# Kernel optimization log

Measured on AMD Instinct MI355X. Metric: run time of the kernel, lower is better.

## Reference

```python
import jax, jax.numpy as jnp
import numpy as np

N = 2048; E = 5; C = 2; W_IN = 256; W_OUT = 128; NUM_CLASS = 8; NT = 1024


def _norm(H, add):
    # faithful to GTN.norm: transpose, zero diagonal, (optionally add I),
    # row-degree-normalize (diag(deg^-1) @ H expressed as row scaling), transpose back
    Ht = H.T
    n = Ht.shape[0]
    eye = jnp.eye(n, dtype=Ht.dtype)
    Ht = Ht * (1.0 - eye)
    if add:
        Ht = Ht + eye
    deg = jnp.sum(Ht, axis=1)
    deg_inv = jnp.where(deg == 0, jnp.zeros_like(deg), 1.0 / deg)
    return (deg_inv[:, None] * Ht).T


def _gtconv(A_e, w):
    # A_e: [E, N, N]; w: [C, E]; softmax over edge types then weighted sum
    return jnp.einsum('ce,enm->cnm', jax.nn.softmax(w, axis=1), A_e)


def setup_inputs() -> dict:
    key = jax.random.key(0)
    ks = jax.random.split(key, 12)
    A = jax.random.uniform(ks[0], (N, N, E), dtype=jnp.float32)
    X = jax.random.uniform(ks[1], (N, W_IN), dtype=jnp.float32)  # BCE target, in [0,1]
    target_x = jax.random.randint(ks[2], (NT,), 0, N)
    target = jax.random.randint(ks[3], (NT,), 0, NUM_CLASS)
    w0a = 0.1 * jax.random.normal(ks[4], (C, E), dtype=jnp.float32)
    w0b = 0.1 * jax.random.normal(ks[5], (C, E), dtype=jnp.float32)
    w1a = 0.1 * jax.random.normal(ks[6], (C, E), dtype=jnp.float32)
    W = jax.random.normal(ks[7], (W_IN, W_OUT), dtype=jnp.float32) * (1.0 / np.sqrt(W_IN))
    W1 = jax.random.normal(ks[8], (W_OUT * C, W_OUT), dtype=jnp.float32) * (1.0 / np.sqrt(W_OUT * C))
    W2 = jax.random.normal(ks[9], (W_OUT * C, W_IN), dtype=jnp.float32) * (1.0 / np.sqrt(W_OUT * C))
    lin_w = jax.random.normal(ks[10], (NUM_CLASS, W_OUT), dtype=jnp.float32) * (1.0 / np.sqrt(W_OUT))
    lin_b = jnp.zeros((NUM_CLASS,), dtype=jnp.float32)
    return {"A": A, "X": X, "W": W, "W1": W1, "W2": W2, "lin_w": lin_w,
            "lin_b": lin_b, "w0a": w0a, "w0b": w0b, "w1a": w1a,
            "target_x": target_x, "target": target}


def reference(A, X, W, W1, W2, lin_w, lin_b, w0a, w0b, w1a, target_x, target):
    A_e = jnp.transpose(A, (2, 0, 1))          # [E, N, N]
    # layer 0 (first=True): H = conv1(A) @ conv2(A)
    a = _gtconv(A_e, w0a)                      # [C, N, N]
    b = _gtconv(A_e, w0b)
    H = jnp.einsum('cij,cjk->cik', a, b)
    # layer 1 (first=False): H = normalization(H) @ conv1(A)
    Hn = jax.vmap(lambda h: _norm(h, False))(H)
    a1 = _gtconv(A_e, w1a)
    H = jnp.einsum('cij,cjk->cik', Hn, a1)
    # per-channel GCN conv: relu(norm(H_c, add=True).T @ (X @ W)), concat on features
    XW = X @ W                                 # [N, w_out]
    Hn2 = jax.vmap(lambda h: _norm(h, True))(H)
    Xc = jax.nn.relu(jnp.einsum('cji,jd->cid', Hn2, XW))  # [C, N, w_out]
    n = X.shape[0]
    X_cat = jnp.transpose(Xc, (1, 0, 2)).reshape(n, -1)   # [N, C*w_out]
    # sum channels, then the two head GCN convs share norm(H_sum, add=True)
    Hs = _norm(jnp.sum(H, axis=0), True)
    X_r = Hs.T @ (X_cat @ W2)                  # [N, w_in]
    X_o = Hs.T @ (X_cat @ W1)                  # [N, w_out]
    y = X_o[target_x] @ lin_w.T + lin_b        # [NT, num_class]
    # clamp reconstruction into [0,1] via sigmoid on out-of-range entries
    X_r = jnp.where(X_r > 1, jax.nn.sigmoid(X_r), X_r)
    X_r = jnp.where(X_r < 0, jax.nn.sigmoid(X_r), X_r)
    p = jnp.clip(X_r, 1e-7, 1.0 - 1e-7)
    lossR = -jnp.mean(X * jnp.log(p) + (1.0 - X) * jnp.log1p(-p))
    logp = jax.nn.log_softmax(y, axis=-1)
    lossC = -jnp.mean(jnp.take_along_axis(logp, target[:, None], axis=1))
    loss = lossC + lossR
    Ws = (jax.lax.stop_gradient(jax.nn.softmax(w0a, axis=1)),
          jax.lax.stop_gradient(jax.nn.softmax(w0b, axis=1)),
          jax.lax.stop_gradient(jax.nn.softmax(w1a, axis=1)))
    return (loss, y, Ws, lossR)
```

## Files before the change

### kernel.cpp

```cpp
#include <hip/hip_runtime.h>
#include <hip/hip_bf16.h>
#include <math.h>

#define NDIM 2048
#define EDIM 5
#define CDIM 2
#define WIN 256
#define WOUT 128
#define NCLS 8
#define NTGT 1024
#define NN ((size_t)NDIM * NDIM)
#define HNSC 256.0f
#define HNSCI 0.00390625f

typedef __attribute__((ext_vector_type(8))) short short8v;
typedef __attribute__((ext_vector_type(4))) float float4v;
typedef __attribute__((ext_vector_type(8))) int int8v;
typedef __attribute__((ext_vector_type(4))) int int4v;
typedef __attribute__((ext_vector_type(2))) int int2v;

__device__ __forceinline__ void gl2lds16(const void* g, void* l) {
  __builtin_amdgcn_global_load_lds((__attribute__((address_space(1))) const unsigned int*)g,
                                   (__attribute__((address_space(3))) unsigned int*)l, 16, 0, 0);
}
__device__ __forceinline__ float bf2f(unsigned short u) {
  return __uint_as_float(((unsigned)u) << 16);
}
__device__ __forceinline__ unsigned short f2bf(float f) {
  __hip_bfloat16 h = __float2bfloat16(f);
  return *(unsigned short*)&h;
}
__device__ __forceinline__ unsigned char f2fp8(float f) {
  return (unsigned char)(__builtin_amdgcn_cvt_pk_fp8_f32(f, f, 0, false) & 0xff);
}

#define N_XC (CDIM * NDIM * WOUT)
#define N_XO (NDIM * 384)
#define N_W12 (2 * WOUT * 384)
#define N_PREP (N_XC + N_XO + N_W12 + CDIM * NDIM + 16 + 30)
__global__ __launch_bounds__(256) void wsum_mega_k(
    const float* __restrict__ A, const float* __restrict__ w0a,
    const float* __restrict__ w0b, const float* __restrict__ w1a,
    unsigned char* __restrict__ a_out, unsigned char* __restrict__ bT,
    unsigned char* __restrict__ a1T,
    float* __restrict__ acc, float* __restrict__ deg,
    float* __restrict__ XcPre, float* __restrict__ XoXr, float* __restrict__ W12,
    const float* __restrict__ W1, const float* __restrict__ W2,
    float* __restrict__ dout) {
  const int b = blockIdx.x;
  const int tid = threadIdx.x;
  if (b >= 4096) {
    int idx = (b - 4096) * 256 + tid;
    if (idx < N_XC) { XcPre[idx] = 0.f; return; }
    idx -= N_XC;
    if (idx < N_XO) { XoXr[idx] = 0.f; return; }
    idx -= N_XO;
    if (idx < N_W12) {
      int k = idx / 384, j = idx - k * 384;
      W12[idx] = (j < 128) ? W1[k * 128 + j] : W2[k * 256 + (j - 128)];
      return;
    }
    idx -= N_W12;
    if (idx < CDIM * NDIM) { deg[idx] = 0.f; return; }
    idx -= CDIM * NDIM;
    if (idx < 16) { acc[idx] = 0.f; return; }
    idx -= 16;
    if (idx < 30) {
      int m = idx / 10, rr = idx - m * 10, c = rr / 5, e = rr - c * 5;
      const float* src = (m == 0) ? w0a : (m == 1) ? w0b : w1a;
      float mx = -1e30f;
      for (int t = 0; t < 5; ++t) mx = fmaxf(mx, src[c * 5 + t]);
      float s = 0.f, ve = 0.f;
      for (int t = 0; t < 5; ++t) {
        float ex = expf(src[c * 5 + t] - mx);
        s += ex;
        if (t == e) ve = ex;
      }
      dout[1 + NTGT * NCLS + idx] = ve / s;
    }
    return;
  }
  __shared__ float swl[32];
  __shared__ float tb[CDIM][32][33];
  __shared__ float tc[CDIM][32][33];
  if (tid < 6) {
    int m = tid >> 1, c = tid & 1;
    const float* src = (m == 0) ? w0a : (m == 1) ? w0b : w1a;
    float mx = -1e30f;
    for (int e = 0; e < 5; ++e) mx = fmaxf(mx, src[c * 5 + e]);
    float ex[5]; float s = 0.f;
    for (int e = 0; e < 5; ++e) { ex[e] = expf(src[c * 5 + e] - mx); s += ex[e]; }
    for (int e = 0; e < 5; ++e) swl[m * 10 + c * 5 + e] = ex[e] / s;
  }
  __syncthreads();
  const int bx = (b & 63) * 32, by = (b >> 6) * 32;
  const int tx = tid & 31, ty = tid >> 5;
#pragma unroll
  for (int rr = 0; rr < 32; rr += 8) {
    int n = by + ty + rr, m = bx + tx;
    size_t base = ((size_t)n * NDIM + m) * EDIM;
    float v0 = A[base], v1 = A[base + 1], v2 = A[base + 2], v3 = A[base + 3], v4 = A[base + 4];
#pragma unroll
    for (int c = 0; c < CDIM; ++c) {
      float sa = swl[c*5]*v0 + swl[c*5+1]*v1 + swl[c*5+2]*v2 + swl[c*5+3]*v3 + swl[c*5+4]*v4;
      float sb = swl[10+c*5]*v0 + swl[10+c*5+1]*v1 + swl[10+c*5+2]*v2 + swl[10+c*5+3]*v3 + swl[10+c*5+4]*v4;
      float sc = swl[20+c*5]*v0 + swl[20+c*5+1]*v1 + swl[20+c*5+2]*v2 + swl[20+c*5+3]*v3 + swl[20+c*5+4]*v4;
      a_out[c * NN + (size_t)n * NDIM + m] = f2fp8(sa);
      tb[c][ty + rr][tx] = sb;
      tc[c][ty + rr][tx] = sc;
    }
  }
  __syncthreads();
#pragma unroll
  for (int rr = 0; rr < 32; rr += 8) {
    int mm = bx + ty + rr, nn2 = by + tx;
#pragma unroll
    for (int c = 0; c < CDIM; ++c) {
      bT[c * NN + (size_t)mm * NDIM + nn2] = f2fp8(tb[c][tx][ty + rr]);
      a1T[c * NN + (size_t)mm * NDIM + nn2] = f2fp8(tc[c][tx][ty + rr]);
    }
  }
}

__global__ __launch_bounds__(256) void mfma_fp8_k(
    const unsigned char* __restrict__ Ab, const unsigned char* __restrict__ Bt,
    __hip_bfloat16* __restrict__ Cv, int K, int ldc,
    size_t sA, size_t sB, size_t sC, float* __restrict__ cs) {
  __shared__ __align__(16) unsigned char As[128 * 128];
  __shared__ __align__(16) unsigned char Bs[128 * 128];
  const int tid = threadIdx.x;
  const int lane = tid & 63;
  const int wave = tid >> 6;
  const int batch = blockIdx.z;
  const unsigned char* A = Ab + (size_t)batch * sA;
  const unsigned char* B = Bt + (size_t)batch * sB;
  const int row0 = blockIdx.y * 128;
  const int col0 = blockIdx.x * 128;

  const int wr = (wave >> 1) * 64;
  const int wc = (wave & 1) * 64;
  const int q = lane >> 4;
  const int r = lane & 15;

  float4v acc[4][4] = {};

  const int srow = lane >> 3;
  const int scol = ((lane & 7) ^ (srow & 7)) * 16;
  const int fsw = r & 7;

  for (int k0 = 0; k0 < K; k0 += 128) {
    __syncthreads();
#pragma unroll
    for (int s = 0; s < 4; ++s) {
      gl2lds16(A + (size_t)(row0 + s * 32 + wave * 8 + srow) * K + k0 + scol,
               As + s * 4096 + wave * 1024);
      gl2lds16(B + (size_t)(col0 + s * 32 + wave * 8 + srow) * K + k0 + scol,
               Bs + s * 4096 + wave * 1024);
    }
    __syncthreads();

    union { int8v v; int4v h[2]; } ua[4], ub[4];
#pragma unroll
    for (int i = 0; i < 4; ++i) {
      const unsigned char* pa = As + (size_t)(wr + i * 16 + r) * 128;
      const unsigned char* pb = Bs + (size_t)(wc + i * 16 + r) * 128;
      ua[i].h[0] = *(const int4v*)(pa + (((2 * q) ^ fsw) * 16));
      ua[i].h[1] = *(const int4v*)(pa + (((2 * q + 1) ^ fsw) * 16));
      ub[i].h[0] = *(const int4v*)(pb + (((2 * q) ^ fsw) * 16));
      ub[i].h[1] = *(const int4v*)(pb + (((2 * q + 1) ^ fsw) * 16));
    }
#pragma unroll
    for (int i = 0; i < 4; ++i)
#pragma unroll
      for (int j = 0; j < 4; ++j)
        acc[i][j] = __builtin_amdgcn_mfma_scale_f32_16x16x128_f8f6f4(
            ua[i].v, ub[j].v, acc[i][j], 0, 0, 0, 0x7F7F7F7F, 0, 0x7F7F7F7F);
  }

  __hip_bfloat16* Cp = Cv + (size_t)batch * sC;
#pragma unroll
  for (int i = 0; i < 4; ++i) {
    int row = row0 + wr + i * 16 + q * 4;
#pragma unroll
    for (int j = 0; j < 4; ++j) {
      int col = col0 + wc + j * 16 + r;
#pragma unroll
      for (int e = 0; e < 4; ++e)
        Cp[(size_t)(row + e) * ldc + col] = __float2bfloat16(acc[i][j][e]);
    }
  }

  if (cs) {
    float* csp = cs + (size_t)batch * NDIM;
#pragma unroll
    for (int j = 0; j < 4; ++j) {
      int col = col0 + wc + j * 16 + r;
      float s = 0.f;
#pragma unroll
      for (int i = 0; i < 4; ++i) {
        int rowb = row0 + wr + i * 16 + q * 4;
#pragma unroll
        for (int e = 0; e < 4; ++e)
          if (rowb + e != col) s += acc[i][j][e];
      }
      s += __shfl_xor(s, 16, 64);
      s += __shfl_xor(s, 32, 64);
      if (lane < 16) atomicAdd(&csp[col], s);
    }
  }
}

__global__ __launch_bounds__(256) void mfma_bt_k(
    const __hip_bfloat16* __restrict__ Ab, const __hip_bfloat16* __restrict__ Bt,
    float* __restrict__ Cv, int K, int ldc,
    size_t sA, size_t sB, size_t sC, int nsplit) {
  __shared__ __hip_bfloat16 As[128 * 64];
  __shared__ __hip_bfloat16 Bs[128 * 64];
  const int tid = threadIdx.x;
  const int lane = tid & 63;
  const int wave = tid >> 6;
  const int batch = blockIdx.z / nsplit;
  const int split = blockIdx.z - batch * nsplit;
  const __hip_bfloat16* A = Ab + (size_t)batch * sA;
  const __hip_bfloat16* B = Bt + (size_t)batch * sB;
  const int row0 = blockIdx.y * 128;
  const int col0 = blockIdx.x * 128;
  const int kchunk = K / nsplit;
  const int kbeg = split * kchunk;
  const int kend = kbeg + kchunk;

  const int wr = (wave >> 1) * 64;
  const int wc = (wave & 1) * 64;
  const int q = lane >> 4;
  const int r = lane & 15;

  float4v acc[4][4] = {};

  const int srow = lane >> 3;
  const int scol = ((lane & 7) ^ (srow & 7)) * 8;
  const int fsw = r & 7;

  for (int k0 = kbeg; k0 < kend; k0 += 64) {
    __syncthreads();
#pragma unroll
    for (int s = 0; s < 4; ++s) {
      gl2lds16(A + (size_t)(row0 + s * 32 + wave * 8 + srow) * K + k0 + scol,
               (char*)As + s * 4096 + wave * 1024);
      gl2lds16(B + (size_t)(col0 + s * 32 + wave * 8 + srow) * K + k0 + scol,
               (char*)Bs + s * 4096 + wave * 1024);
    }
    __syncthreads();
#pragma unroll
    for (int h = 0; h < 2; ++h) {
      short8v af[4], bf[4];
#pragma unroll
      for (int i = 0; i < 4; ++i) {
        af[i] = *(const short8v*)((const char*)As + (size_t)(wr + i * 16 + r) * 128 +
                                  (((h * 4 + q) ^ fsw) * 16));
        bf[i] = *(const short8v*)((const char*)Bs + (size_t)(wc + i * 16 + r) * 128 +
                                  (((h * 4 + q) ^ fsw) * 16));
      }
#pragma unroll
      for (int i = 0; i < 4; ++i)
#pragma unroll
        for (int j = 0; j < 4; ++j)
          acc[i][j] = __builtin_amdgcn_mfma_f32_16x16x32_bf16(af[i], bf[j], acc[i][j], 0, 0, 0);
    }
  }

  float* Cp = Cv + (size_t)batch * sC;
#pragma unroll
  for (int i = 0; i < 4; ++i) {
    int row = row0 + wr + i * 16 + q * 4;
#pragma unroll
    for (int j = 0; j < 4; ++j) {
      int col = col0 + wc + j * 16 + r;
#pragma unroll
      for (int e = 0; e < 4; ++e) {
        float v = acc[i][j][e];
        if (nsplit > 1) atomicAdd(&Cp[(size_t)(row + e) * ldc + col], v);
        else Cp[(size_t)(row + e) * ldc + col] = v;
      }
    }
  }
}

__global__ __launch_bounds__(256) void col_scale_k(const __hip_bfloat16* __restrict__ H,
                                                   const float* __restrict__ deg,
                                                   unsigned char* __restrict__ out) {
  size_t base = ((size_t)blockIdx.x * 256 + threadIdx.x) * 8;
  int c = (int)(base >> 22);
  int i = (int)((base >> 11) & (NDIM - 1));
  int j0 = (int)(base & (NDIM - 1));
  union { short8v v; unsigned short u[8]; } p;
  p.v = *(const short8v*)(H + base);
  float f[8];
#pragma unroll
  for (int t = 0; t < 8; ++t) {
    int j = j0 + t;
    float d = deg[c * NDIM + j];
    float inv = (d == 0.f) ? 0.f : HNSC / d;
    float v = (i == j) ? 0.f : bf2f(p.u[t]);
    f[t] = v * inv;
  }
  int w0 = __builtin_amdgcn_cvt_pk_fp8_f32(f[0], f[1], 0, false);
  w0 = __builtin_amdgcn_cvt_pk_fp8_f32(f[2], f[3], w0, true);
  int w1 = __builtin_amdgcn_cvt_pk_fp8_f32(f[4], f[5], 0, false);
  w1 = __builtin_amdgcn_cvt_pk_fp8_f32(f[6], f[7], w1, true);
  int2v o; o.x = w0; o.y = w1;
  *(int2v*)(out + base) = o;
}

__global__ __launch_bounds__(256) void rowmega_k(const __hip_bfloat16* __restrict__ H1T,
                                                 __hip_bfloat16* __restrict__ Hn2T,
                                                 __hip_bfloat16* __restrict__ HsT) {
  const int m = blockIdx.x;
  const int tid = threadIdx.x;
  const size_t rb = (size_t)m * NDIM + tid * 8;
  union { short8v v; unsigned short u[8]; } a0, a1;
  a0.v = *(const short8v*)(H1T + rb);
  a1.v = *(const short8v*)(H1T + NN + rb);
  float v0[8], v1[8];
  float s0 = 0.f, s1 = 0.f;
#pragma unroll
  for (int t = 0; t < 8; ++t) {
    v0[t] = bf2f(a0.u[t]) * HNSCI;
    v1[t] = bf2f(a1.u[t]) * HNSCI;
    s0 += v0[t]; s1 += v1[t];
  }
  __shared__ float ds[2];
  __shared__ float red[2][4];
  __shared__ float bc[3];
  if (tid == (m >> 3)) { ds[0] = v0[m & 7]; ds[1] = v1[m & 7]; }
  for (int off = 32; off > 0; off >>= 1) {
    s0 += __shfl_down(s0, off, 64);
    s1 += __shfl_down(s1, off, 64);
  }
  if ((tid & 63) == 0) { red[0][tid >> 6] = s0; red[1][tid >> 6] = s1; }
  __syncthreads();
  if (tid == 0) {
    float t0 = red[0][0] + red[0][1] + red[0][2] + red[0][3];
    float t1 = red[1][0] + red[1][1] + red[1][2] + red[1][3];
    float r0 = t0 - ds[0] + 1.f;
    float r1 = t1 - ds[1] + 1.f;
    float rs = t0 + t1 - ds[0] - ds[1] + 1.f;
    bc[0] = (r0 == 0.f) ? 0.f : 1.f / r0;
    bc[1] = (r1 == 0.f) ? 0.f : 1.f / r1;
    bc[2] = (rs == 0.f) ? 0.f : 1.f / rs;
  }
  __syncthreads();
  float i0 = bc[0], i1 = bc[1], is = bc[2];
  union { short8v v; unsigned short u[8]; } o0, o1, os;
#pragma unroll
  for (int t = 0; t < 8; ++t) {
    bool dg = (tid * 8 + t == m);
    o0.u[t] = f2bf((dg ? 1.f : v0[t]) * i0);
    o1.u[t] = f2bf((dg ? 1.f : v1[t]) * i1);
    os.u[t] = f2bf((dg ? 1.f : (v0[t] + v1[t])) * is);
  }
  *(short8v*)(Hn2T + rb) = o0.v;
  *(short8v*)(Hn2T + NN + rb) = o1.v;
  *(short8v*)(HsT + rb) = os.v;
}

#define TS 64
#define BK 16
__global__ __launch_bounds__(256) void sgemm_tb_k(const float* __restrict__ A,
                                                  const float* __restrict__ B,
                                                  __hip_bfloat16* __restrict__ Dt,
                                                  int K, int lda, int ldb, int ldt,
                                                  int amode) {
  __shared__ float As[BK][TS];
  __shared__ float Bs[BK][TS + 4];
  const int tid = threadIdx.x;
  const int brow = blockIdx.y * TS;
  const int bcol = blockIdx.x * TS;
  const int tx = tid & 15;
  const int ty = tid >> 4;
  const int la_r = tid >> 2;
  const int la_k = (tid & 3) << 2;
  const int lb_k = tid >> 4;
  const int lb_c = (tid & 15) << 2;
  float acc[4][4] = {{0.f}};
  for (int k0 = 0; k0 < K; k0 += BK) {
    float4 av;
    if (amode == 0) {
      av = *(const float4*)(A + (size_t)(brow + la_r) * lda + k0 + la_k);
    } else {
      int k = k0 + la_k;
      const float* ap = A + (size_t)(k >> 7) * ((size_t)NDIM * WOUT) +
                        (size_t)(brow + la_r) * WOUT + (k & 127);
      av = *(const float4*)ap;
      av.x = fmaxf(av.x, 0.f); av.y = fmaxf(av.y, 0.f);
      av.z = fmaxf(av.z, 0.f); av.w = fmaxf(av.w, 0.f);
    }
    float4 bv = *(const float4*)(B + (size_t)(k0 + lb_k) * ldb + bcol + lb_c);
    __syncthreads();
    As[la_k + 0][la_r] = av.x;
    As[la_k + 1][la_r] = av.y;
    As[la_k + 2][la_r] = av.z;
    As[la_k + 3][la_r] = av.w;
    *(float4*)&Bs[lb_k][lb_c] = bv;
    __syncthreads();
#pragma unroll
    for (int kk = 0; kk < BK; ++kk) {
      float a0 = As[kk][ty * 4 + 0], a1 = As[kk][ty * 4 + 1];
      float a2 = As[kk][ty * 4 + 2], a3 = As[kk][ty * 4 + 3];
      float b0 = Bs[kk][tx * 4 + 0], b1 = Bs[kk][tx * 4 + 1];
      float b2 = Bs[kk][tx * 4 + 2], b3 = Bs[kk][tx * 4 + 3];
      acc[0][0] += a0 * b0; acc[0][1] += a0 * b1; acc[0][2] += a0 * b2; acc[0][3] += a0 * b3;
      acc[1][0] += a1 * b0; acc[1][1] += a1 * b1; acc[1][2] += a1 * b2; acc[1][3] += a1 * b3;
      acc[2][0] += a2 * b0; acc[2][1] += a2 * b1; acc[2][2] += a2 * b2; acc[2][3] += a2 * b3;
      acc[3][0] += a3 * b0; acc[3][1] += a3 * b1; acc[3][2] += a3 * b2; acc[3][3] += a3 * b3;
    }
  }
#pragma unroll
  for (int i = 0; i < 4; ++i)
#pragma unroll
    for (int j = 0; j < 4; ++j)
      Dt[(size_t)(bcol + tx * 4 + j) * ldt + brow + ty * 4 + i] = __float2bfloat16(acc[i][j]);
}

__global__ __launch_bounds__(256) void loss_mega_k(const float* __restrict__ XoXr,
                                                   const float* __restrict__ X,
                                                   const float* __restrict__ lin_w,
                                                   const float* __restrict__ lin_b,
                                                   const int* __restrict__ txs,
                                                   const int* __restrict__ tgt,
                                                   float* __restrict__ yout,
                                                   float* __restrict__ acc) {
  const int b = blockIdx.x;
  const int tid = threadIdx.x;
  if (b < 2048) {
    float xr = XoXr[(size_t)b * 384 + 128 + tid];
    if (xr > 1.f) xr = 1.f / (1.f + expf(-xr));
    if (xr < 0.f) xr = 1.f / (1.f + expf(-xr));
    float p = fminf(fmaxf(xr, 1e-7f), 1.f - 1e-7f);
    float xv = X[(size_t)b * WIN + tid];
    float t = xv * logf(p) + (1.f - xv) * log1pf(-p);
    for (int off = 32; off > 0; off >>= 1) t += __shfl_down(t, off, 64);
    __shared__ float red[4];
    if ((tid & 63) == 0) red[tid >> 6] = t;
    __syncthreads();
    if (tid == 0) atomicAdd(acc + 1, red[0] + red[1] + red[2] + red[3]);
    return;
  }
  const int t = b - 2048;
  __shared__ float xo[WOUT];
  __shared__ float ys[NCLS];
  int x = txs[t];
  if (tid < WOUT) xo[tid] = XoXr[(size_t)x * 384 + tid];
  __syncthreads();
  if (tid < NCLS) {
    float s = lin_b[tid];
    for (int d = 0; d < WOUT; ++d) s += xo[d] * lin_w[tid * WOUT + d];
    ys[tid] = s;
    yout[(size_t)t * NCLS + tid] = s;
  }
  __syncthreads();
  if (tid == 0) {
    float m = ys[0];
    for (int k = 1; k < NCLS; ++k) m = fmaxf(m, ys[k]);
    float se = 0.f;
    for (int k = 0; k < NCLS; ++k) se += expf(ys[k] - m);
    float lse = m + logf(se);
    atomicAdd(acc, lse - ys[tgt[t]]);
  }
}

__global__ void finalize_k(const float* __restrict__ acc, float* __restrict__ dout) {
  float lossC = acc[0] / (float)NTGT;
  float lossR = -acc[1] / (float)(NDIM * WIN);
  dout[0] = lossC + lossR;
  dout[1 + NTGT * NCLS + 30] = lossR;
}

extern "C" void kernel_launch(void* const* d_in, const int* in_sizes, int n_in,
                              void* d_out, int out_size, void* d_ws, size_t ws_size,
                              hipStream_t stream) {
  const float* A    = (const float*)d_in[0];
  const float* X    = (const float*)d_in[1];
  const float* W    = (const float*)d_in[2];
  const float* W1   = (const float*)d_in[3];
  const float* W2   = (const float*)d_in[4];
  const float* linw = (const float*)d_in[5];
  const float* linb = (const float*)d_in[6];
  const float* w0a  = (const float*)d_in[7];
  const float* w0b  = (const float*)d_in[8];
  const float* w1a  = (const float*)d_in[9];
  const int* txs    = (const int*)d_in[10];
  const int* tgt    = (const int*)d_in[11];
  float* dout = (float*)d_out;

  float* ws = (float*)d_ws;
  unsigned char* wb = (unsigned char*)d_ws;
  unsigned char* P_a   = wb;
  unsigned char* P_bT  = wb + 2 * NN;
  unsigned char* P_a1T = wb + 4 * NN;
  unsigned char* P_Hn  = wb + 6 * NN;
  __hip_bfloat16* H_bf   = (__hip_bfloat16*)(ws + 2 * NN);
  __hip_bfloat16* H1T_bf = (__hip_bfloat16*)(ws + 3 * NN);
  __hip_bfloat16* Hn2T   = (__hip_bfloat16*)(ws + 4 * NN);
  __hip_bfloat16* HsT    = (__hip_bfloat16*)(ws);
  float* sm   = ws + 5 * NN;
  float* acc   = sm;                 sm += 16;
  float* deg   = sm;                 sm += CDIM * NDIM;
  __hip_bfloat16* XWT = (__hip_bfloat16*)sm;    sm += (size_t)NDIM * WOUT / 2;
  float* XcPre = sm;                 sm += (size_t)CDIM * NDIM * WOUT;
  float* W12   = sm;                 sm += (size_t)(2 * WOUT) * 384;
  __hip_bfloat16* XC12T = (__hip_bfloat16*)sm;  sm += (size_t)NDIM * 384 / 2;
  float* XoXr  = sm;                 sm += (size_t)NDIM * 384;

  dim3 blk256(256);

  wsum_mega_k<<<dim3(4096 + (N_PREP + 255) / 256), blk256, 0, stream>>>(
      A, w0a, w0b, w1a, P_a, P_bT, P_a1T, acc, deg, XcPre, XoXr, W12, W1, W2, dout);
  mfma_fp8_k<<<dim3(16, 16, 2), blk256, 0, stream>>>(P_a, P_bT, H_bf, NDIM, NDIM,
                                                     NN, NN, NN, deg);
  col_scale_k<<<dim3((unsigned)(2 * NN / 2048)), blk256, 0, stream>>>(H_bf, deg, P_Hn);
  mfma_fp8_k<<<dim3(16, 16, 2), blk256, 0, stream>>>(P_a1T, P_Hn, H1T_bf, NDIM, NDIM,
                                                     NN, NN, NN, nullptr);
  rowmega_k<<<dim3(NDIM), blk256, 0, stream>>>(H1T_bf, Hn2T, HsT);
  sgemm_tb_k<<<dim3(WOUT / TS, NDIM / TS), blk256, 0, stream>>>(X, W, XWT, WIN,
                                                                WIN, WOUT, NDIM, 0);
  mfma_bt_k<<<dim3(1, 16, 16), blk256, 0, stream>>>(Hn2T, XWT, XcPre, NDIM, WOUT,
                                                    NN, 0, (size_t)NDIM * WOUT, 8);
  sgemm_tb_k<<<dim3(384 / TS, NDIM / TS), blk256, 0, stream>>>(XcPre, W12, XC12T, 2 * WOUT,
                                                               0, 384, NDIM, 1);
  mfma_bt_k<<<dim3(3, 16, 8), blk256, 0, stream>>>(HsT, XC12T, XoXr, NDIM, 384,
                                                   0, 0, 0, 8);
  loss_mega_k<<<dim3(2048 + NTGT), blk256, 0, stream>>>(XoXr, X, linw, linb, txs, tgt,
                                                        dout + 1, acc);
  finalize_k<<<dim3(1), dim3(1), 0, stream>>>(acc, dout);
}
```

Baseline: 341.7 us.

## Replace fp32 SIMT GEMMs with bf16 MFMA and split-K partial buffers

The two small fp32 SIMT GEMMs (X@W and Xcat@W12) are replaced by the bf16 MFMA kernel, with operands converted and transposed to bf16 in the prep kernel. Split-K results are written to separate per-split partial buffers instead of atomically added, so consumers (a new reduce+relu kernel and the loss kernel) sum the partials. This removes the float atomics and the zero-init passes. In exchange it adds an extra kernel launch, extra partial-buffer traffic, and bf16 rounding of X and the weights.

```diff
diff --git a/kernel.cpp b/kernel.cpp
--- a/kernel.cpp
+++ b/kernel.cpp
@@ -34,33 +34,39 @@
   return (unsigned char)(__builtin_amdgcn_cvt_pk_fp8_f32(f, f, 0, false) & 0xff);
 }
 
-#define N_XC (CDIM * NDIM * WOUT)
-#define N_XO (NDIM * 384)
-#define N_W12 (2 * WOUT * 384)
-#define N_PREP (N_XC + N_XO + N_W12 + CDIM * NDIM + 16 + 30)
+#define N_XBF (NDIM * WIN)
+#define N_WT (WIN * WOUT)
+#define N_W12T (384 * WIN)
+#define N_PREP (N_XBF + N_WT + N_W12T + CDIM * NDIM + 16 + 30)
 __global__ __launch_bounds__(256) void wsum_mega_k(
     const float* __restrict__ A, const float* __restrict__ w0a,
     const float* __restrict__ w0b, const float* __restrict__ w1a,
     unsigned char* __restrict__ a_out, unsigned char* __restrict__ bT,
     unsigned char* __restrict__ a1T,
     float* __restrict__ acc, float* __restrict__ deg,
-    float* __restrict__ XcPre, float* __restrict__ XoXr, float* __restrict__ W12,
+    const float* __restrict__ X, const float* __restrict__ W,
     const float* __restrict__ W1, const float* __restrict__ W2,
+    __hip_bfloat16* __restrict__ Xbf, __hip_bfloat16* __restrict__ WTbf,
+    __hip_bfloat16* __restrict__ W12Tbf,
     float* __restrict__ dout) {
   const int b = blockIdx.x;
   const int tid = threadIdx.x;
   if (b >= 4096) {
     int idx = (b - 4096) * 256 + tid;
-    if (idx < N_XC) { XcPre[idx] = 0.f; return; }
-    idx -= N_XC;
-    if (idx < N_XO) { XoXr[idx] = 0.f; return; }
-    idx -= N_XO;
-    if (idx < N_W12) {
-      int k = idx / 384, j = idx - k * 384;
-      W12[idx] = (j < 128) ? W1[k * 128 + j] : W2[k * 256 + (j - 128)];
+    if (idx < N_XBF) { Xbf[idx] = __float2bfloat16(X[idx]); return; }
+    idx -= N_XBF;
+    if (idx < N_WT) {
+      int d = idx >> 8, k = idx & 255;
+      WTbf[idx] = __float2bfloat16(W[k * WOUT + d]);
       return;
     }
-    idx -= N_W12;
+    idx -= N_WT;
+    if (idx < N_W12T) {
+      int j = idx >> 8, k = idx & 255;
+      W12Tbf[idx] = __float2bfloat16(j < 128 ? W1[k * 128 + j] : W2[k * 256 + (j - 128)]);
+      return;
+    }
+    idx -= N_W12T;
     if (idx < CDIM * NDIM) { deg[idx] = 0.f; return; }
     idx -= CDIM * NDIM;
     if (idx < 16) { acc[idx] = 0.f; return; }
@@ -212,8 +218,8 @@
 
 __global__ __launch_bounds__(256) void mfma_bt_k(
     const __hip_bfloat16* __restrict__ Ab, const __hip_bfloat16* __restrict__ Bt,
-    float* __restrict__ Cv, int K, int ldc,
-    size_t sA, size_t sB, size_t sC, int nsplit) {
+    void* __restrict__ Cv, int K, int ldc,
+    size_t sA, size_t sB, size_t sC, size_t sSplit, int nsplit, int mode) {
   __shared__ __hip_bfloat16 As[128 * 64];
   __shared__ __hip_bfloat16 Bs[128 * 64];
   const int tid = threadIdx.x;
@@ -268,18 +274,30 @@
     }
   }
 
-  float* Cp = Cv + (size_t)batch * sC;
-#pragma unroll
-  for (int i = 0; i < 4; ++i) {
-    int row = row0 + wr + i * 16 + q * 4;
-#pragma unroll
-    for (int j = 0; j < 4; ++j) {
-      int col = col0 + wc + j * 16 + r;
-#pragma unroll
-      for (int e = 0; e < 4; ++e) {
-        float v = acc[i][j][e];
-        if (nsplit > 1) atomicAdd(&Cp[(size_t)(row + e) * ldc + col], v);
-        else Cp[(size_t)(row + e) * ldc + col] = v;
+  if (mode == 1) {
+    __hip_bfloat16* Cp = (__hip_bfloat16*)Cv + (size_t)batch * sC;
+#pragma unroll
+    for (int i = 0; i < 4; ++i) {
+      int row = row0 + wr + i * 16 + q * 4;
+#pragma unroll
+      for (int j = 0; j < 4; ++j) {
+        int col = col0 + wc + j * 16 + r;
+#pragma unroll
+        for (int e = 0; e < 4; ++e)
+          Cp[(size_t)(row + e) * ldc + col] = __float2bfloat16(acc[i][j][e]);
+      }
+    }
+  } else {
+    float* Cp = (float*)Cv + (size_t)batch * sC + (size_t)split * sSplit;
+#pragma unroll
+    for (int i = 0; i < 4; ++i) {
+      int row = row0 + wr + i * 16 + q * 4;
+#pragma unroll
+      for (int j = 0; j < 4; ++j) {
+        int col = col0 + wc + j * 16 + r;
+#pragma unroll
+        for (int e = 0; e < 4; ++e)
+          Cp[(size_t)(row + e) * ldc + col] = acc[i][j][e];
       }
     }
   }
@@ -363,65 +381,20 @@
   *(short8v*)(HsT + rb) = os.v;
 }
 
-#define TS 64
-#define BK 16
-__global__ __launch_bounds__(256) void sgemm_tb_k(const float* __restrict__ A,
-                                                  const float* __restrict__ B,
-                                                  __hip_bfloat16* __restrict__ Dt,
-                                                  int K, int lda, int ldb, int ldt,
-                                                  int amode) {
-  __shared__ float As[BK][TS];
-  __shared__ float Bs[BK][TS + 4];
-  const int tid = threadIdx.x;
-  const int brow = blockIdx.y * TS;
-  const int bcol = blockIdx.x * TS;
-  const int tx = tid & 15;
-  const int ty = tid >> 4;
-  const int la_r = tid >> 2;
-  const int la_k = (tid & 3) << 2;
-  const int lb_k = tid >> 4;
-  const int lb_c = (tid & 15) << 2;
-  float acc[4][4] = {{0.f}};
-  for (int k0 = 0; k0 < K; k0 += BK) {
-    float4 av;
-    if (amode == 0) {
-      av = *(const float4*)(A + (size_t)(brow + la_r) * lda + k0 + la_k);
-    } else {
-      int k = k0 + la_k;
-      const float* ap = A + (size_t)(k >> 7) * ((size_t)NDIM * WOUT) +
-                        (size_t)(brow + la_r) * WOUT + (k & 127);
-      av = *(const float4*)ap;
-      av.x = fmaxf(av.x, 0.f); av.y = fmaxf(av.y, 0.f);
-      av.z = fmaxf(av.z, 0.f); av.w = fmaxf(av.w, 0.f);
-    }
-    float4 bv = *(const float4*)(B + (size_t)(k0 + lb_k) * ldb + bcol + lb_c);
-    __syncthreads();
-    As[la_k + 0][la_r] = av.x;
-    As[la_k + 1][la_r] = av.y;
-    As[la_k + 2][la_r] = av.z;
-    As[la_k + 3][la_r] = av.w;
-    *(float4*)&Bs[lb_k][lb_c] = bv;
-    __syncthreads();
-#pragma unroll
-    for (int kk = 0; kk < BK; ++kk) {
-      float a0 = As[kk][ty * 4 + 0], a1 = As[kk][ty * 4 + 1];
-      float a2 = As[kk][ty * 4 + 2], a3 = As[kk][ty * 4 + 3];
-      float b0 = Bs[kk][tx * 4 + 0], b1 = Bs[kk][tx * 4 + 1];
-      float b2 = Bs[kk][tx * 4 + 2], b3 = Bs[kk][tx * 4 + 3];
-      acc[0][0] += a0 * b0; acc[0][1] += a0 * b1; acc[0][2] += a0 * b2; acc[0][3] += a0 * b3;
-      acc[1][0] += a1 * b0; acc[1][1] += a1 * b1; acc[1][2] += a1 * b2; acc[1][3] += a1 * b3;
-      acc[2][0] += a2 * b0; acc[2][1] += a2 * b1; acc[2][2] += a2 * b2; acc[2][3] += a2 * b3;
-      acc[3][0] += a3 * b0; acc[3][1] += a3 * b1; acc[3][2] += a3 * b2; acc[3][3] += a3 * b3;
-    }
-  }
-#pragma unroll
-  for (int i = 0; i < 4; ++i)
-#pragma unroll
-    for (int j = 0; j < 4; ++j)
-      Dt[(size_t)(bcol + tx * 4 + j) * ldt + brow + ty * 4 + i] = __float2bfloat16(acc[i][j]);
-}
-
-__global__ __launch_bounds__(256) void loss_mega_k(const float* __restrict__ XoXr,
+__global__ __launch_bounds__(256) void reduce_relu_k(const float* __restrict__ P7,
+                                                     __hip_bfloat16* __restrict__ Xcat) {
+  int idx = blockIdx.x * 256 + threadIdx.x;
+  int c = idx >> 18;
+  int rem = idx & 262143;
+  float s = 0.f;
+#pragma unroll
+  for (int sp = 0; sp < 8; ++sp)
+    s += P7[(size_t)c * 2097152 + (size_t)sp * 262144 + rem];
+  int n = rem >> 7, d = rem & 127;
+  Xcat[(size_t)n * 256 + (c << 7) + d] = __float2bfloat16(fmaxf(s, 0.f));
+}
+
+__global__ __launch_bounds__(256) void loss_mega_k(const float* __restrict__ P10,
                                                    const float* __restrict__ X,
                                                    const float* __restrict__ lin_w,
                                                    const float* __restrict__ lin_b,
@@ -432,7 +405,10 @@
   const int b = blockIdx.x;
   const int tid = threadIdx.x;
   if (b < 2048) {
-    float xr = XoXr[(size_t)b * 384 + 128 + tid];
+    float xr = 0.f;
+#pragma unroll
+    for (int sp = 0; sp < 8; ++sp)
+      xr += P10[(size_t)sp * 786432 + (size_t)b * 384 + 128 + tid];
     if (xr > 1.f) xr = 1.f / (1.f + expf(-xr));
     if (xr < 0.f) xr = 1.f / (1.f + expf(-xr));
     float p = fminf(fmaxf(xr, 1e-7f), 1.f - 1e-7f);
@@ -449,7 +425,13 @@
   __shared__ float xo[WOUT];
   __shared__ float ys[NCLS];
   int x = txs[t];
-  if (tid < WOUT) xo[tid] = XoXr[(size_t)x * 384 + tid];
+  if (tid < WOUT) {
+    float s = 0.f;
+#pragma unroll
+    for (int sp = 0; sp < 8; ++sp)
+      s += P10[(size_t)sp * 786432 + (size_t)x * 384 + tid];
+    xo[tid] = s;
+  }
   __syncthreads();
   if (tid < NCLS) {
     float s = lin_b[tid];
@@ -505,31 +487,36 @@
   float* sm   = ws + 5 * NN;
   float* acc   = sm;                 sm += 16;
   float* deg   = sm;                 sm += CDIM * NDIM;
-  __hip_bfloat16* XWT = (__hip_bfloat16*)sm;    sm += (size_t)NDIM * WOUT / 2;
-  float* XcPre = sm;                 sm += (size_t)CDIM * NDIM * WOUT;
-  float* W12   = sm;                 sm += (size_t)(2 * WOUT) * 384;
-  __hip_bfloat16* XC12T = (__hip_bfloat16*)sm;  sm += (size_t)NDIM * 384 / 2;
-  float* XoXr  = sm;                 sm += (size_t)NDIM * 384;
+  __hip_bfloat16* Xbf    = (__hip_bfloat16*)sm;  sm += N_XBF / 2;
+  __hip_bfloat16* WTbf   = (__hip_bfloat16*)sm;  sm += N_WT / 2;
+  __hip_bfloat16* W12Tbf = (__hip_bfloat16*)sm;  sm += N_W12T / 2;
+  __hip_bfloat16* XWT    = (__hip_bfloat16*)sm;  sm += (size_t)WOUT * NDIM / 2;
+  __hip_bfloat16* Xcat   = (__hip_bfloat16*)sm;  sm += (size_t)NDIM * 256 / 2;
+  __hip_bfloat16* XC12T  = (__hip_bfloat16*)sm;  sm += (size_t)384 * NDIM / 2;
+  float* P7   = sm;                  sm += (size_t)16 * 262144;
+  float* P10  = sm;                  sm += (size_t)8 * 786432;
 
   dim3 blk256(256);
 
   wsum_mega_k<<<dim3(4096 + (N_PREP + 255) / 256), blk256, 0, stream>>>(
-      A, w0a, w0b, w1a, P_a, P_bT, P_a1T, acc, deg, XcPre, XoXr, W12, W1, W2, dout);
+      A, w0a, w0b, w1a, P_a, P_bT, P_a1T, acc, deg, X, W, W1, W2,
+      Xbf, WTbf, W12Tbf, dout);
   mfma_fp8_k<<<dim3(16, 16, 2), blk256, 0, stream>>>(P_a, P_bT, H_bf, NDIM, NDIM,
                                                      NN, NN, NN, deg);
   col_scale_k<<<dim3((unsigned)(2 * NN / 2048)), blk256, 0, stream>>>(H_bf, deg, P_Hn);
   mfma_fp8_k<<<dim3(16, 16, 2), blk256, 0, stream>>>(P_a1T, P_Hn, H1T_bf, NDIM, NDIM,
                                                      NN, NN, NN, nullptr);
   rowmega_k<<<dim3(NDIM), blk256, 0, stream>>>(H1T_bf, Hn2T, HsT);
-  sgemm_tb_k<<<dim3(WOUT / TS, NDIM / TS), blk256, 0, stream>>>(X, W, XWT, WIN,
-                                                                WIN, WOUT, NDIM, 0);
-  mfma_bt_k<<<dim3(1, 16, 16), blk256, 0, stream>>>(Hn2T, XWT, XcPre, NDIM, WOUT,
-                                                    NN, 0, (size_t)NDIM * WOUT, 8);
-  sgemm_tb_k<<<dim3(384 / TS, NDIM / TS), blk256, 0, stream>>>(XcPre, W12, XC12T, 2 * WOUT,
-                                                               0, 384, NDIM, 1);
-  mfma_bt_k<<<dim3(3, 16, 8), blk256, 0, stream>>>(HsT, XC12T, XoXr, NDIM, 384,
-                                                   0, 0, 0, 8);
-  loss_mega_k<<<dim3(2048 + NTGT), blk256, 0, stream>>>(XoXr, X, linw, linb, txs, tgt,
+  mfma_bt_k<<<dim3(16, 1, 1), blk256, 0, stream>>>(WTbf, Xbf, XWT, WIN, NDIM,
+                                                   0, 0, 0, 0, 1, 1);
+  mfma_bt_k<<<dim3(1, 16, 16), blk256, 0, stream>>>(Hn2T, XWT, P7, NDIM, WOUT,
+                                                    NN, 0, 2097152, 262144, 8, 2);
+  reduce_relu_k<<<dim3(2048), blk256, 0, stream>>>(P7, Xcat);
+  mfma_bt_k<<<dim3(16, 3, 1), blk256, 0, stream>>>(W12Tbf, Xcat, XC12T, 256, NDIM,
+                                                   0, 0, 0, 0, 1, 1);
+  mfma_bt_k<<<dim3(3, 16, 8), blk256, 0, stream>>>(HsT, XC12T, P10, NDIM, 384,
+                                                   0, 0, 0, 786432, 8, 2);
+  loss_mega_k<<<dim3(2048 + NTGT), blk256, 0, stream>>>(P10, X, linw, linb, txs, tgt,
                                                         dout + 1, acc);
   finalize_k<<<dim3(1), dim3(1), 0, stream>>>(acc, dout);
 }
```

Result: faster. 300.1 us (-12.2%).
